# Performance work log

Measured on AMD Instinct MI355X. Metric: run time of the kernel, lower is better.

Reference implementation:

```python
import jax, jax.numpy as jnp
import numpy as np

MARGIN = 1.0
EPS = 1e-8


def setup_inputs() -> dict:
    key = jax.random.key(0)
    k1, k2 = jax.random.split(key)
    B, D, NUM_CLASSES = 8192, 512, 100
    features = jax.random.normal(k1, (B, D), dtype=jnp.float32)
    labels = jax.random.randint(k2, (B,), 0, NUM_CLASSES, dtype=jnp.int64)
    return {"features": features, "labels": labels}


def _metric_tensor(features):
    # G = I + feature covariance (curvature-aware metric on the feature manifold)
    B, D = features.shape
    centered = features - jnp.mean(features, axis=0, keepdims=True)
    cov = jnp.einsum('bi,bj->ij', centered, centered) / jnp.float32(B)
    return jnp.eye(D, dtype=features.dtype) + cov


def _masked_random_idx(mask, key):
    # gumbel-max trick: uniform random index among True entries of each row of mask [B,B]
    g = -jnp.log(-jnp.log(jax.random.uniform(key, mask.shape, dtype=jnp.float32) + EPS) + EPS)
    scores = jnp.where(mask, g, -jnp.inf)
    return jnp.argmax(scores, axis=1)


def reference(features, labels):
    B = features.shape[0]
    G = _metric_tensor(features)

    same = labels[:, None] == labels[None, :]              # [B,B]
    not_self = ~jnp.eye(B, dtype=bool)
    pos_mask = same & not_self
    neg_mask = ~same

    kp, kn = jax.random.split(jax.random.key(42))
    pos_idx = _masked_random_idx(pos_mask, kp)             # [B]
    neg_idx = _masked_random_idx(neg_mask, kn)             # [B]
    valid = jnp.any(pos_mask, axis=1) & jnp.any(neg_mask, axis=1)

    diff_p = features - features[pos_idx]                  # [B,D]
    diff_n = features - features[neg_idx]                  # [B,D]
    # Riemannian distance: sqrt((x-y)^T G (x-y))
    d_pos = jnp.sqrt(jnp.einsum('bi,ij,bj->b', diff_p, G, diff_p) + EPS)
    d_neg = jnp.sqrt(jnp.einsum('bi,ij,bj->b', diff_n, G, diff_n) + EPS)

    per_sample = jnp.maximum(d_pos - d_neg + MARGIN, 0.0)
    per_sample = jnp.where(valid, per_sample, 0.0)
    n_valid = jnp.maximum(jnp.sum(valid.astype(jnp.float32)), 1.0)
    return jnp.sum(per_sample) / n_valid
```

## Files before the change

kernel.cpp:

```cpp
#include <hip/hip_runtime.h>
#include <stdint.h>

#define BSZ   8192
#define DIM   512

typedef __attribute__((ext_vector_type(8))) short short8;
typedef __attribute__((ext_vector_type(4))) float f32x4;
typedef __attribute__((ext_vector_type(8))) uint16_t u16x8;

__host__ __device__ inline uint16_t f2bf(float x) {
  uint32_t u = __float_as_uint(x);
  return (uint16_t)((u + 0x7FFFu + ((u >> 16) & 1u)) >> 16);
}
__host__ __device__ inline float bf2f(uint16_t h) {
  return __uint_as_float(((uint32_t)h) << 16);
}

__host__ __device__ inline uint32_t rotl32(uint32_t v, int s) {
#if defined(__HIP_DEVICE_COMPILE__) && __has_builtin(__builtin_amdgcn_alignbit)
  return __builtin_amdgcn_alignbit(v, v, 32 - s);
#else
  return (v << s) | (v >> (32 - s));
#endif
}

__host__ __device__ inline void threefry2x32(uint32_t k0, uint32_t k1,
                                             uint32_t x0, uint32_t x1,
                                             uint32_t& o0, uint32_t& o1) {
  uint32_t ks2 = k0 ^ k1 ^ 0x1BD11BDAu;
  x0 += k0; x1 += k1;
  x0 += x1; x1 = rotl32(x1, 13); x1 ^= x0;
  x0 += x1; x1 = rotl32(x1, 15); x1 ^= x0;
  x0 += x1; x1 = rotl32(x1, 26); x1 ^= x0;
  x0 += x1; x1 = rotl32(x1,  6); x1 ^= x0;
  x0 += k1; x1 += ks2 + 1u;
  x0 += x1; x1 = rotl32(x1, 17); x1 ^= x0;
  x0 += x1; x1 = rotl32(x1, 29); x1 ^= x0;
  x0 += x1; x1 = rotl32(x1, 16); x1 ^= x0;
  x0 += x1; x1 = rotl32(x1, 24); x1 ^= x0;
  x0 += ks2; x1 += k0 + 2u;
  x0 += x1; x1 = rotl32(x1, 13); x1 ^= x0;
  x0 += x1; x1 = rotl32(x1, 15); x1 ^= x0;
  x0 += x1; x1 = rotl32(x1, 26); x1 ^= x0;
  x0 += x1; x1 = rotl32(x1,  6); x1 ^= x0;
  x0 += k0; x1 += k1 + 3u;
  x0 += x1; x1 = rotl32(x1, 17); x1 ^= x0;
  x0 += x1; x1 = rotl32(x1, 29); x1 ^= x0;
  x0 += x1; x1 = rotl32(x1, 16); x1 ^= x0;
  x0 += x1; x1 = rotl32(x1, 24); x1 ^= x0;
  x0 += k1; x1 += ks2 + 4u;
  x0 += x1; x1 = rotl32(x1, 13); x1 ^= x0;
  x0 += x1; x1 = rotl32(x1, 15); x1 ^= x0;
  x0 += x1; x1 = rotl32(x1, 26); x1 ^= x0;
  x0 += x1; x1 = rotl32(x1,  6); x1 ^= x0;
  x0 += ks2; x1 += k0 + 5u;
  o0 = x0; o1 = x1;
}

constexpr size_t OFF_CTR    = 0;
constexpr size_t OFF_S      = 1024;
constexpr size_t OFF_BSTART = 3072;
constexpr size_t OFF_BIDX   = 4096;
constexpr size_t OFF_PIDX   = 36864;
constexpr size_t OFF_NIDX   = 69632;
constexpr size_t OFF_LPART  = 102400;
constexpr size_t OFF_GB     = 131072;
constexpr size_t OFF_FB     = 2097152;
constexpr size_t OFF_HB     = 10485760;
constexpr size_t ZERO_BYTES = 3072;

__global__ __launch_bounds__(256) void prep_kernel(const float* __restrict__ F,
                                                   uint16_t* __restrict__ Fb,
                                                   float* __restrict__ S) {
  int i = (blockIdx.x * 256 + threadIdx.x) * 8;
  float4 a = *(const float4*)&F[i];
  float4 b = *(const float4*)&F[i + 4];
  u16x8 o;
  o[0] = f2bf(a.x); o[1] = f2bf(a.y); o[2] = f2bf(a.z); o[3] = f2bf(a.w);
  o[4] = f2bf(b.x); o[5] = f2bf(b.y); o[6] = f2bf(b.z); o[7] = f2bf(b.w);
  *(u16x8*)&Fb[i] = o;
  if (blockIdx.x < 256) {
    int b0 = blockIdx.x * 32;
    int t = threadIdx.x;
    float s0 = 0.f, s1 = 0.f;
    for (int r = 0; r < 32; ++r) {
      const float* row = F + (size_t)(b0 + r) * DIM;
      s0 += row[t];
      s1 += row[t + 256];
    }
    atomicAdd(&S[t], s0);
    atomicAdd(&S[t + 256], s1);
  }
}

union CovShared {
  struct { uint16_t sA[64][40]; uint16_t sB[64][40]; } mm;
  struct { int cnt[128]; int base[128]; } bk;
};

__global__ __launch_bounds__(256) void covmat_bucket_kernel(
    const uint16_t* __restrict__ Fb, float* __restrict__ Mpart,
    const int* __restrict__ labels, int* __restrict__ bucketStart,
    int* __restrict__ bucketIdx) {
  __shared__ CovShared sh;
  int bid = blockIdx.x, tid = threadIdx.x;
  if (bid < 256) {
    int chunk = bid & 3;
    int tile = bid >> 2;
    int i0 = (tile >> 3) * 64, j0 = (tile & 7) * 64;
    int kc0 = chunk * 2048;
    int lane = tid & 63, wid = tid >> 6, quad = lane >> 4, l16 = lane & 15;
    int wm = (wid >> 1) * 32, wn = (wid & 1) * 32;
    int sk = tid & 31, sm = (tid >> 5) * 8;
    f32x4 acc[2][2] = {};
    for (int kk = 0; kk < 2048; kk += 32) {
      int krow = kc0 + kk + sk;
      u16x8 va = *(const u16x8*)&Fb[(size_t)krow * DIM + i0 + sm];
      u16x8 vb = *(const u16x8*)&Fb[(size_t)krow * DIM + j0 + sm];
      __syncthreads();
#pragma unroll
      for (int jj = 0; jj < 8; ++jj) { sh.mm.sA[sm + jj][sk] = va[jj]; sh.mm.sB[sm + jj][sk] = vb[jj]; }
      __syncthreads();
#pragma unroll
      for (int r = 0; r < 2; ++r) {
        short8 af = *(short8*)&sh.mm.sA[wm + r * 16 + l16][quad * 8];
#pragma unroll
        for (int c = 0; c < 2; ++c) {
          short8 bf = *(short8*)&sh.mm.sB[wn + c * 16 + l16][quad * 8];
          acc[r][c] = __builtin_amdgcn_mfma_f32_16x16x32_bf16(af, bf, acc[r][c], 0, 0, 0);
        }
      }
    }
    float* outp = Mpart + (size_t)chunk * DIM * DIM;
#pragma unroll
    for (int r = 0; r < 2; ++r)
#pragma unroll
      for (int c = 0; c < 2; ++c)
#pragma unroll
        for (int g = 0; g < 4; ++g)
          outp[(size_t)(i0 + wm + r * 16 + quad * 4 + g) * DIM + j0 + wn + c * 16 + l16] = acc[r][c][g];
  } else {
    if (tid < 128) sh.bk.cnt[tid] = 0;
    __syncthreads();
    for (int b = tid; b < BSZ; b += 256) atomicAdd(&sh.bk.cnt[labels[b]], 1);
    __syncthreads();
    if (tid == 0) {
      int run = 0;
      for (int c = 0; c < 100; ++c) { sh.bk.base[c] = run; bucketStart[c] = run; run += sh.bk.cnt[c]; }
      bucketStart[100] = run;
    }
    __syncthreads();
    for (int b = tid; b < BSZ; b += 256) {
      int p = atomicAdd(&sh.bk.base[labels[b]], 1);
      bucketIdx[p] = b;
    }
  }
}

__global__ __launch_bounds__(256) void buildG_kernel(const float* __restrict__ Mpart,
                                                     const float* __restrict__ S,
                                                     uint16_t* __restrict__ Gb) {
  int idx = blockIdx.x * 256 + threadIdx.x;
  int i = idx >> 9, j = idx & 511;
  float m = Mpart[idx] + Mpart[(size_t)DIM * DIM + idx] +
            Mpart[2 * (size_t)DIM * DIM + idx] + Mpart[3 * (size_t)DIM * DIM + idx];
  const float invB = 1.0f / (float)BSZ;
  float mi = S[i] * invB, mj = S[j] * invB;
  Gb[idx] = f2bf(m * invB - mi * mj + (i == j ? 1.0f : 0.0f));
}

struct SharedMM  { uint16_t sA[128][72]; uint16_t sB[64][72]; };
struct SharedNeg { uint8_t slab[BSZ]; unsigned long long wmax[4]; int curRow; };
union __align__(16) SharedU { SharedMM mm; SharedNeg neg; };

__global__ __launch_bounds__(256) void overlap_kernel(
    const uint16_t* __restrict__ Fb, const uint16_t* __restrict__ Gb,
    uint16_t* __restrict__ Hb, const int* __restrict__ labels,
    const int* __restrict__ bStart, const int* __restrict__ bIdx,
    int* __restrict__ posIdx, int* __restrict__ negIdx,
    int* __restrict__ rowCtr,
    uint32_t kp0, uint32_t kp1, uint32_t kn0, uint32_t kn1) {
  __shared__ SharedU sh;
  int bid = blockIdx.x, tid = threadIdx.x;
  int lane = tid & 63, wid = tid >> 6, quad = lane >> 4, l16 = lane & 15;

  if (bid < 224) {
    int am = tid & 127, ah = (tid >> 7) * 32;
    int bk = tid >> 2, bn = (tid & 3) * 16;
    int tm = wid * 32;
    for (int t = bid; t < 512; t += 224) {
      int n0 = (t & 7) * 64;
      int m0 = (t >> 3) * 128;
      f32x4 acc[2][4] = {};
      for (int k0 = 0; k0 < DIM; k0 += 64) {
        {
          const uint16_t* src = &Fb[(size_t)(m0 + am) * DIM + k0 + ah];
#pragma unroll
          for (int v = 0; v < 4; ++v)
            *(u16x8*)&sh.mm.sA[am][ah + v * 8] = *(const u16x8*)&src[v * 8];
        }
        {
          u16x8 g0 = *(const u16x8*)&Gb[(size_t)(k0 + bk) * DIM + n0 + bn];
          u16x8 g1 = *(const u16x8*)&Gb[(size_t)(k0 + bk) * DIM + n0 + bn + 8];
#pragma unroll
          for (int jj = 0; jj < 8; ++jj) { sh.mm.sB[bn + jj][bk] = g0[jj]; sh.mm.sB[bn + 8 + jj][bk] = g1[jj]; }
        }
        __syncthreads();
#pragma unroll
        for (int k32 = 0; k32 < 64; k32 += 32) {
          short8 af[2];
#pragma unroll
          for (int r = 0; r < 2; ++r)
            af[r] = *(short8*)&sh.mm.sA[tm + r * 16 + l16][k32 + quad * 8];
#pragma unroll
          for (int c = 0; c < 4; ++c) {
            short8 bf = *(short8*)&sh.mm.sB[c * 16 + l16][k32 + quad * 8];
#pragma unroll
            for (int r = 0; r < 2; ++r)
              acc[r][c] = __builtin_amdgcn_mfma_f32_16x16x32_bf16(af[r], bf, acc[r][c], 0, 0, 0);
          }
        }
        __syncthreads();
      }
#pragma unroll
      for (int r = 0; r < 2; ++r)
#pragma unroll
        for (int c = 0; c < 4; ++c)
#pragma unroll
          for (int g = 0; g < 4; ++g)
            Hb[(size_t)(m0 + tm + r * 16 + quad * 4 + g) * DIM + n0 + c * 16 + l16] = f2bf(acc[r][c][g]);
    }
    __syncthreads();
  } else if (bid < 256) {
    for (int row = (bid - 224) * 4 + wid; row < BSZ; row += 128) {
      int cls = labels[row];
      int s = bStart[cls], e = bStart[cls + 1];
      uint32_t base = (uint32_t)(row << 13);
      unsigned long long best = 0;
      for (int t2 = s + lane; t2 < e; t2 += 64) {
        int cc = bIdx[t2];
        uint32_t a0, a1;
        threefry2x32(kp0, kp1, 0u, base + (uint32_t)cc, a0, a1);
        unsigned long long comp = ((unsigned long long)((a0 ^ a1) >> 9) << 32) | (uint32_t)(~cc);
        if (cc == row) comp = 0;
        if (comp > best) best = comp;
      }
#pragma unroll
      for (int off = 32; off; off >>= 1) {
        unsigned long long o = __shfl_down(best, off);
        if (o > best) best = o;
      }
      if (lane == 0) posIdx[row] = best ? (int)(~(uint32_t)best) : -1;
    }
    __syncthreads();
  }

  {
    uint32_t* s32 = (uint32_t*)sh.neg.slab;
#pragma unroll
    for (int pass = 0; pass < 8; ++pass) {
      int idx = pass * 1024 + tid * 4;
      int4 l4 = *(const int4*)&labels[idx];
      uint32_t packed = (uint32_t)(l4.x & 0xFF) | ((uint32_t)(l4.y & 0xFF) << 8) |
                        ((uint32_t)(l4.z & 0xFF) << 16) | ((uint32_t)(l4.w & 0xFF) << 24);
      s32[pass * 256 + tid] = packed;
    }
  }
  __syncthreads();
  while (true) {
    if (tid == 0) sh.neg.curRow = atomicAdd(rowCtr, 1);
    __syncthreads();
    int row = sh.neg.curRow;
    if (row >= BSZ) break;
    uint32_t li = sh.neg.slab[row];
    uint32_t base = (uint32_t)(row << 13);
    unsigned long long bA = 0, bB = 0, bC = 0, bD = 0;
#pragma unroll 2
    for (int it = 0; it < 8; ++it) {
      int c0 = tid + (it << 10);
      int c1 = c0 + 256, c2 = c0 + 512, c3 = c0 + 768;
      uint32_t l0 = sh.neg.slab[c0], l1 = sh.neg.slab[c1], l2 = sh.neg.slab[c2], l3 = sh.neg.slab[c3];
      uint32_t a0, a1, e0, e1, f0, f1, g0, g1;
      threefry2x32(kn0, kn1, 0u, base + (uint32_t)c0, a0, a1);
      threefry2x32(kn0, kn1, 0u, base + (uint32_t)c1, e0, e1);
      threefry2x32(kn0, kn1, 0u, base + (uint32_t)c2, f0, f1);
      threefry2x32(kn0, kn1, 0u, base + (uint32_t)c3, g0, g1);
      unsigned long long compA = ((unsigned long long)((a0 ^ a1) >> 9) << 32) | (uint32_t)(~c0);
      unsigned long long compB = ((unsigned long long)((e0 ^ e1) >> 9) << 32) | (uint32_t)(~c1);
      unsigned long long compC = ((unsigned long long)((f0 ^ f1) >> 9) << 32) | (uint32_t)(~c2);
      unsigned long long compD = ((unsigned long long)((g0 ^ g1) >> 9) << 32) | (uint32_t)(~c3);
      if (l0 == li) compA = 0;
      if (l1 == li) compB = 0;
      if (l2 == li) compC = 0;
      if (l3 == li) compD = 0;
      if (compA > bA) bA = compA;
      if (compB > bB) bB = compB;
      if (compC > bC) bC = compC;
      if (compD > bD) bD = compD;
    }
    if (bB > bA) bA = bB;
    if (bC > bA) bA = bC;
    if (bD > bA) bA = bD;
    unsigned long long best = bA;
#pragma unroll
    for (int off = 32; off; off >>= 1) {
      unsigned long long o = __shfl_down(best, off);
      if (o > best) best = o;
    }
    if (lane == 0) sh.neg.wmax[wid] = best;
    __syncthreads();
    if (tid == 0) {
      best = sh.neg.wmax[0];
      for (int w = 1; w < 4; ++w) if (sh.neg.wmax[w] > best) best = sh.neg.wmax[w];
      negIdx[row] = best ? (int)(~(uint32_t)best) : -1;
    }
    __syncthreads();
  }
}

__global__ __launch_bounds__(256) void loss_kernel(
    const uint16_t* __restrict__ Fb, const uint16_t* __restrict__ Hb,
    const int* __restrict__ posIdx, const int* __restrict__ negIdx,
    float2* __restrict__ lossPart) {
  __shared__ float2 part[4];
  int row = blockIdx.x * 4 + (threadIdx.x >> 6);
  int lane = threadIdx.x & 63;
  int p = posIdx[row], n = negIdx[row];
  bool valid = (p >= 0) && (n >= 0);
  int ps = valid ? p : row;
  int ns = valid ? n : row;
  int k = lane * 8;
  u16x8 f_i = *(const u16x8*)(Fb + (size_t)row * DIM + k);
  u16x8 f_p = *(const u16x8*)(Fb + (size_t)ps * DIM + k);
  u16x8 f_n = *(const u16x8*)(Fb + (size_t)ns * DIM + k);
  u16x8 h_i = *(const u16x8*)(Hb + (size_t)row * DIM + k);
  u16x8 h_p = *(const u16x8*)(Hb + (size_t)ps * DIM + k);
  u16x8 h_n = *(const u16x8*)(Hb + (size_t)ns * DIM + k);
  float qii = 0.f, qpp = 0.f, qip = 0.f, qnn = 0.f, qin = 0.f;
#pragma unroll
  for (int jj = 0; jj < 8; ++jj) {
    float fi = bf2f(f_i[jj]), fp = bf2f(f_p[jj]), fn = bf2f(f_n[jj]);
    float hi = bf2f(h_i[jj]), hp = bf2f(h_p[jj]), hn = bf2f(h_n[jj]);
    qii += fi * hi;
    qpp += fp * hp;
    qip += fi * hp;
    qnn += fn * hn;
    qin += fi * hn;
  }
#pragma unroll
  for (int off = 32; off > 0; off >>= 1) {
    qii += __shfl_down(qii, off);
    qpp += __shfl_down(qpp, off);
    qip += __shfl_down(qip, off);
    qnn += __shfl_down(qnn, off);
    qin += __shfl_down(qin, off);
  }
  if (lane == 0) {
    float d2p = fmaxf(qii + qpp - 2.f * qip, 0.f);
    float d2n = fmaxf(qii + qnn - 2.f * qin, 0.f);
    float v = fmaxf(sqrtf(d2p + 1e-8f) - sqrtf(d2n + 1e-8f) + 1.0f, 0.0f);
    if (!valid) v = 0.f;
    part[threadIdx.x >> 6] = make_float2(v, valid ? 1.f : 0.f);
  }
  __syncthreads();
  if (threadIdx.x == 0) {
    float s = 0.f, c = 0.f;
#pragma unroll
    for (int w = 0; w < 4; ++w) { s += part[w].x; c += part[w].y; }
    lossPart[blockIdx.x] = make_float2(s, c);
  }
}

__global__ __launch_bounds__(256) void finalize_kernel(const float2* __restrict__ lossPart,
                                                       float* __restrict__ out) {
  __shared__ float2 wsum[4];
  int tid = threadIdx.x;
  float s = 0.f, c = 0.f;
  for (int z = tid; z < 2048; z += 256) {
    float2 v = lossPart[z];
    s += v.x; c += v.y;
  }
#pragma unroll
  for (int off = 32; off > 0; off >>= 1) {
    s += __shfl_down(s, off);
    c += __shfl_down(c, off);
  }
  if ((tid & 63) == 0) wsum[tid >> 6] = make_float2(s, c);
  __syncthreads();
  if (tid == 0) {
    s = 0.f; c = 0.f;
#pragma unroll
    for (int w = 0; w < 4; ++w) { s += wsum[w].x; c += wsum[w].y; }
    out[0] = s / fmaxf(c, 1.0f);
  }
}

extern "C" void kernel_launch(void* const* d_in, const int* in_sizes, int n_in,
                              void* d_out, int out_size, void* d_ws, size_t ws_size,
                              hipStream_t stream) {
  const float* F = (const float*)d_in[0];
  const int* labels = (const int*)d_in[1];
  float* out = (float*)d_out;
  char* ws = (char*)d_ws;

  int* rowCtr    = (int*)(ws + OFF_CTR);
  float* S       = (float*)(ws + OFF_S);
  int* bStart    = (int*)(ws + OFF_BSTART);
  int* bIdx      = (int*)(ws + OFF_BIDX);
  int* posIdx    = (int*)(ws + OFF_PIDX);
  int* negIdx    = (int*)(ws + OFF_NIDX);
  float2* lPart  = (float2*)(ws + OFF_LPART);
  uint16_t* Gb   = (uint16_t*)(ws + OFF_GB);
  uint16_t* Fb   = (uint16_t*)(ws + OFF_FB);
  uint16_t* Hb   = (uint16_t*)(ws + OFF_HB);
  float* Mpart   = (float*)(ws + OFF_HB);

  uint32_t kp0, kp1, kn0, kn1;
  threefry2x32(0u, 42u, 0u, 0u, kp0, kp1);
  threefry2x32(0u, 42u, 0u, 1u, kn0, kn1);

  hipMemsetAsync(ws, 0, ZERO_BYTES, stream);

  prep_kernel<<<2048, 256, 0, stream>>>(F, Fb, S);

  covmat_bucket_kernel<<<257, 256, 0, stream>>>(Fb, Mpart, labels, bStart, bIdx);

  buildG_kernel<<<(DIM * DIM) / 256, 256, 0, stream>>>(Mpart, S, Gb);

  overlap_kernel<<<1024, 256, 0, stream>>>(Fb, Gb, Hb, labels, bStart, bIdx,
                                           posIdx, negIdx, rowCtr,
                                           kp0, kp1, kn0, kn1);

  loss_kernel<<<BSZ / 4, 256, 0, stream>>>(Fb, Hb, posIdx, negIdx, lPart);

  finalize_kernel<<<1, 256, 0, stream>>>(lPart, out);
}
```

Before: 313.3 us.

## Split negative-sampling rows into half-row chunks with striped counters and atomicMax

The negative-index search now hands out half-row chunks from four striped atomic counters, in place of one global row counter. Partial maxima are merged with a 64-bit atomicMax into a zeroed neg64 array, which prep_kernel clears, and the loss kernel decodes the index from it. Separately, the covariance split-K is doubled from 4 to 8 K-chunks (513 blocks), and buildG reduces 8 partials. This is meant to cut counter contention, give the dynamic scheduler finer-grained work, and raise covariance occupancy. In exchange it adds extra atomics, extra partial-sum traffic, and Mpart now needs 8 MB of workspace.

Measured after the change: 385.1 us. 22.9% more time.

```diff
diff --git a/kernel.cpp b/kernel.cpp
--- a/kernel.cpp
+++ b/kernel.cpp
@@ -62,16 +62,17 @@
 constexpr size_t OFF_BSTART = 3072;
 constexpr size_t OFF_BIDX   = 4096;
 constexpr size_t OFF_PIDX   = 36864;
-constexpr size_t OFF_NIDX   = 69632;
-constexpr size_t OFF_LPART  = 102400;
-constexpr size_t OFF_GB     = 131072;
+constexpr size_t OFF_NEG64  = 69632;
+constexpr size_t OFF_LPART  = 135168;
+constexpr size_t OFF_GB     = 163840;
 constexpr size_t OFF_FB     = 2097152;
 constexpr size_t OFF_HB     = 10485760;
 constexpr size_t ZERO_BYTES = 3072;
 
 __global__ __launch_bounds__(256) void prep_kernel(const float* __restrict__ F,
                                                    uint16_t* __restrict__ Fb,
-                                                   float* __restrict__ S) {
+                                                   float* __restrict__ S,
+                                                   unsigned long long* __restrict__ neg64) {
   int i = (blockIdx.x * 256 + threadIdx.x) * 8;
   float4 a = *(const float4*)&F[i];
   float4 b = *(const float4*)&F[i + 4];
@@ -79,6 +80,7 @@
   o[0] = f2bf(a.x); o[1] = f2bf(a.y); o[2] = f2bf(a.z); o[3] = f2bf(a.w);
   o[4] = f2bf(b.x); o[5] = f2bf(b.y); o[6] = f2bf(b.z); o[7] = f2bf(b.w);
   *(u16x8*)&Fb[i] = o;
+  if (blockIdx.x < 32) neg64[blockIdx.x * 256 + threadIdx.x] = 0ull;
   if (blockIdx.x < 256) {
     int b0 = blockIdx.x * 32;
     int t = threadIdx.x;
@@ -104,16 +106,16 @@
     int* __restrict__ bucketIdx) {
   __shared__ CovShared sh;
   int bid = blockIdx.x, tid = threadIdx.x;
-  if (bid < 256) {
-    int chunk = bid & 3;
-    int tile = bid >> 2;
+  if (bid < 512) {
+    int chunk = bid & 7;
+    int tile = bid >> 3;
     int i0 = (tile >> 3) * 64, j0 = (tile & 7) * 64;
-    int kc0 = chunk * 2048;
+    int kc0 = chunk * 1024;
     int lane = tid & 63, wid = tid >> 6, quad = lane >> 4, l16 = lane & 15;
     int wm = (wid >> 1) * 32, wn = (wid & 1) * 32;
     int sk = tid & 31, sm = (tid >> 5) * 8;
     f32x4 acc[2][2] = {};
-    for (int kk = 0; kk < 2048; kk += 32) {
+    for (int kk = 0; kk < 1024; kk += 32) {
       int krow = kc0 + kk + sk;
       u16x8 va = *(const u16x8*)&Fb[(size_t)krow * DIM + i0 + sm];
       u16x8 vb = *(const u16x8*)&Fb[(size_t)krow * DIM + j0 + sm];
@@ -162,23 +164,36 @@
                                                      uint16_t* __restrict__ Gb) {
   int idx = blockIdx.x * 256 + threadIdx.x;
   int i = idx >> 9, j = idx & 511;
-  float m = Mpart[idx] + Mpart[(size_t)DIM * DIM + idx] +
-            Mpart[2 * (size_t)DIM * DIM + idx] + Mpart[3 * (size_t)DIM * DIM + idx];
+  float m = 0.f;
+#pragma unroll
+  for (int z = 0; z < 8; ++z) m += Mpart[(size_t)z * DIM * DIM + idx];
   const float invB = 1.0f / (float)BSZ;
   float mi = S[i] * invB, mj = S[j] * invB;
   Gb[idx] = f2bf(m * invB - mi * mj + (i == j ? 1.0f : 0.0f));
 }
 
 struct SharedMM  { uint16_t sA[128][72]; uint16_t sB[64][72]; };
-struct SharedNeg { uint8_t slab[BSZ]; unsigned long long wmax[4]; int curRow; };
+struct SharedNeg { uint8_t slab[BSZ]; unsigned long long wmax[4]; int nextChunk; };
 union __align__(16) SharedU { SharedMM mm; SharedNeg neg; };
+
+__device__ inline int grab_chunk(int* ctrs, int myc, uint32_t& exh) {
+#pragma unroll
+  for (int t = 0; t < 4; ++t) {
+    int ci = (myc + t) & 3;
+    if (exh & (1u << ci)) continue;
+    int v = atomicAdd(&ctrs[ci], 1);
+    if (v < 4096) return ci * 4096 + v;
+    exh |= 1u << ci;
+  }
+  return -1;
+}
 
 __global__ __launch_bounds__(256) void overlap_kernel(
     const uint16_t* __restrict__ Fb, const uint16_t* __restrict__ Gb,
     uint16_t* __restrict__ Hb, const int* __restrict__ labels,
     const int* __restrict__ bStart, const int* __restrict__ bIdx,
-    int* __restrict__ posIdx, int* __restrict__ negIdx,
-    int* __restrict__ rowCtr,
+    int* __restrict__ posIdx, unsigned long long* __restrict__ neg64,
+    int* __restrict__ ctrs,
     uint32_t kp0, uint32_t kp1, uint32_t kn0, uint32_t kn1) {
   __shared__ SharedU sh;
   int bid = blockIdx.x, tid = threadIdx.x;
@@ -266,18 +281,22 @@
       s32[pass * 256 + tid] = packed;
     }
   }
+  uint32_t exh = 0;
+  if (tid == 0) sh.neg.nextChunk = grab_chunk(ctrs, bid & 3, exh);
   __syncthreads();
   while (true) {
-    if (tid == 0) sh.neg.curRow = atomicAdd(rowCtr, 1);
-    __syncthreads();
-    int row = sh.neg.curRow;
-    if (row >= BSZ) break;
+    int cur = sh.neg.nextChunk;
+    __syncthreads();
+    if (cur < 0) break;
+    if (tid == 0) sh.neg.nextChunk = grab_chunk(ctrs, bid & 3, exh);
+    int row = cur >> 1;
+    int colbase = (cur & 1) << 12;
     uint32_t li = sh.neg.slab[row];
     uint32_t base = (uint32_t)(row << 13);
     unsigned long long bA = 0, bB = 0, bC = 0, bD = 0;
 #pragma unroll 2
-    for (int it = 0; it < 8; ++it) {
-      int c0 = tid + (it << 10);
+    for (int it = 0; it < 4; ++it) {
+      int c0 = colbase + tid + (it << 10);
       int c1 = c0 + 256, c2 = c0 + 512, c3 = c0 + 768;
       uint32_t l0 = sh.neg.slab[c0], l1 = sh.neg.slab[c1], l2 = sh.neg.slab[c2], l3 = sh.neg.slab[c3];
       uint32_t a0, a1, e0, e1, f0, f1, g0, g1;
@@ -312,7 +331,7 @@
     if (tid == 0) {
       best = sh.neg.wmax[0];
       for (int w = 1; w < 4; ++w) if (sh.neg.wmax[w] > best) best = sh.neg.wmax[w];
-      negIdx[row] = best ? (int)(~(uint32_t)best) : -1;
+      if (best) atomicMax(&neg64[row], best);
     }
     __syncthreads();
   }
@@ -320,15 +339,16 @@
 
 __global__ __launch_bounds__(256) void loss_kernel(
     const uint16_t* __restrict__ Fb, const uint16_t* __restrict__ Hb,
-    const int* __restrict__ posIdx, const int* __restrict__ negIdx,
+    const int* __restrict__ posIdx, const unsigned long long* __restrict__ neg64,
     float2* __restrict__ lossPart) {
   __shared__ float2 part[4];
   int row = blockIdx.x * 4 + (threadIdx.x >> 6);
   int lane = threadIdx.x & 63;
-  int p = posIdx[row], n = negIdx[row];
-  bool valid = (p >= 0) && (n >= 0);
+  int p = posIdx[row];
+  unsigned long long nv = neg64[row];
+  bool valid = (p >= 0) && (nv != 0ull);
   int ps = valid ? p : row;
-  int ns = valid ? n : row;
+  int ns = valid ? (int)(~(uint32_t)nv) : row;
   int k = lane * 8;
   u16x8 f_i = *(const u16x8*)(Fb + (size_t)row * DIM + k);
   u16x8 f_p = *(const u16x8*)(Fb + (size_t)ps * DIM + k);
@@ -403,12 +423,12 @@
   float* out = (float*)d_out;
   char* ws = (char*)d_ws;
 
-  int* rowCtr    = (int*)(ws + OFF_CTR);
+  int* ctrs      = (int*)(ws + OFF_CTR);
   float* S       = (float*)(ws + OFF_S);
   int* bStart    = (int*)(ws + OFF_BSTART);
   int* bIdx      = (int*)(ws + OFF_BIDX);
   int* posIdx    = (int*)(ws + OFF_PIDX);
-  int* negIdx    = (int*)(ws + OFF_NIDX);
+  unsigned long long* neg64 = (unsigned long long*)(ws + OFF_NEG64);
   float2* lPart  = (float2*)(ws + OFF_LPART);
   uint16_t* Gb   = (uint16_t*)(ws + OFF_GB);
   uint16_t* Fb   = (uint16_t*)(ws + OFF_FB);
@@ -421,17 +441,17 @@
 
   hipMemsetAsync(ws, 0, ZERO_BYTES, stream);
 
-  prep_kernel<<<2048, 256, 0, stream>>>(F, Fb, S);
-
-  covmat_bucket_kernel<<<257, 256, 0, stream>>>(Fb, Mpart, labels, bStart, bIdx);
+  prep_kernel<<<2048, 256, 0, stream>>>(F, Fb, S, neg64);
+
+  covmat_bucket_kernel<<<513, 256, 0, stream>>>(Fb, Mpart, labels, bStart, bIdx);
 
   buildG_kernel<<<(DIM * DIM) / 256, 256, 0, stream>>>(Mpart, S, Gb);
 
   overlap_kernel<<<1024, 256, 0, stream>>>(Fb, Gb, Hb, labels, bStart, bIdx,
-                                           posIdx, negIdx, rowCtr,
+                                           posIdx, neg64, ctrs,
                                            kp0, kp1, kn0, kn1);
 
-  loss_kernel<<<BSZ / 4, 256, 0, stream>>>(Fb, Hb, posIdx, negIdx, lPart);
+  loss_kernel<<<BSZ / 4, 256, 0, stream>>>(Fb, Hb, posIdx, neg64, lPart);
 
   finalize_kernel<<<1, 256, 0, stream>>>(lPart, out);
 }
```
